# Kernel tuning notes

Measured on AMD Instinct MI355X. Metric: run time of the kernel, lower is better.

Reference implementation:

```python
import jax, jax.numpy as jnp
import numpy as np

NE, EW, TOP_K, T_D, MAXNNZ = 32, 2944, 4, 8, 256
ALPHA, LIMIT, ORIG = 1.702, 7.0, 2880
HID = 2048


def setup_inputs() -> dict:
    key = jax.random.key(0)
    ks = jax.random.split(key, 7)
    dt = jnp.float16
    hid = jax.random.normal(ks[0], (1, 1024, HID), dtype=dt)
    # rand_init() sets all params to torch.rand(...)/5 -> Uniform[0, 0.2)
    gate_w = (jax.random.uniform(ks[1], (NE, HID), dtype=dt) * 0.2).astype(dt)
    u = (jax.random.uniform(ks[2], (NE * EW, HID), dtype=dt) * 0.2).astype(dt)
    g = (jax.random.uniform(ks[3], (NE * EW, HID), dtype=dt) * 0.2).astype(dt)
    d = (jax.random.uniform(ks[4], (HID, NE * EW), dtype=dt) * 0.2).astype(dt)
    ub = (jax.random.uniform(ks[5], (NE * EW,), dtype=dt) * 0.2).astype(dt)
    gb = (jax.random.uniform(ks[6], (NE * EW,), dtype=dt) * 0.2).astype(dt)
    return {"hid": hid, "gate_w": gate_w, "u": u, "g": g, "d": d, "ub": ub, "gb": gb}


def _act(up, gate):
    # clamped GLU: gate clamped above, up clamped both sides; glu = g*sigmoid(alpha*g); (up+1)*glu
    gate = jnp.minimum(gate, LIMIT)
    up = jnp.clip(up, -LIMIT, LIMIT)
    glu = gate * jax.nn.sigmoid(gate * ALPHA)
    act = (up + 1.0) * glu
    return act.at[..., ORIG:].set(0)  # padded inter dims (2880..2944) zeroed


def _forward(hid, gate_w, u, g, d, ub, gb):
    B, S, H = hid.shape
    x = hid.reshape(-1, H)           # [bs, H]
    bs = x.shape[0]

    # --- routing: softmax -> top-k -> renormalize -> scatter to sparse weights ---
    logits = (x @ gate_w.T).astype(jnp.float32)          # [bs, NE]
    probs = jax.nn.softmax(logits, axis=1)
    vals, idx = jax.lax.top_k(probs, TOP_K)
    vals = vals / vals.sum(axis=1, keepdims=True)
    sparse_rw = jnp.zeros_like(probs).at[jnp.arange(bs)[:, None], idx].set(vals)
    rw = sparse_rw.astype(x.dtype)                        # [bs, NE]

    # --- expert selection: t_d dense experts + t_d sparse experts by load ---
    routing_n = jnp.count_nonzero(rw, axis=0)
    mask_c = jax.lax.top_k(routing_n, 2 * T_D)[1]         # [2*T_D]
    cd, cs = mask_c[:T_D], mask_c[T_D:]
    # top-MAXNNZ tokens per sparse expert
    mask_r = jax.lax.top_k(sparse_rw[:, cs].T, MAXNNZ)[1].T  # [MAXNNZ, T_D]

    U = u.reshape(NE, EW, H)
    G = g.reshape(NE, EW, H)
    UB = ub.reshape(NE, EW)
    GB = gb.reshape(NE, EW)
    D = d.reshape(H, NE, EW)

    # --- dense experts: every token runs through the t_d hottest experts ---
    up_d = jnp.einsum('nh,teh->nte', x, U[cd]) + UB[cd]   # [bs, T_D, EW]
    gt_d = jnp.einsum('nh,teh->nte', x, G[cd]) + GB[cd]
    act_d = _act(up_d, gt_d) * rw[:, cd][..., None]       # routing weight combine
    out = jnp.einsum('nte,hte->nh', act_d, D[:, cd])      # [bs, H]

    # --- sparse experts: gather top-MAXNNZ tokens, MLP, scatter-add back ---
    xs = x[mask_r]                                        # [M, T_D, H]
    up_s = jnp.einsum('mth,teh->mte', xs, U[cs]) + UB[cs]
    gt_s = jnp.einsum('mth,teh->mte', xs, G[cs]) + GB[cs]
    w_s = rw[mask_r, cs[None, :]]                         # [M, T_D]
    act_s = _act(up_s, gt_s) * w_s[..., None]
    contrib = jnp.einsum('mte,hte->mth', act_s, D[:, cs])  # [M, T_D, H]
    out = out.at[mask_r.reshape(-1)].add(contrib.reshape(-1, H))

    return out.reshape(B, S, H)


def reference(hid, gate_w, u, g, d, ub, gb):
    return _forward(hid, gate_w, u, g, d, ub, gb)
```

## Files before the change

kernel.cpp:

```cpp
#include <hip/hip_runtime.h>

#define HID 2048
#define NE_ 32
#define EW_ 2944
#define ORIG_ 2880
#define TOPK_ 4
#define MAXNNZ_ 256
#define BS_ 1024
#define NEWTOT (NE_*EW_)

typedef unsigned short u16;
typedef _Float16 h8  __attribute__((ext_vector_type(8)));
typedef float  f32x4 __attribute__((ext_vector_type(4)));
typedef float  fv4   __attribute__((ext_vector_type(4)));

__device__ __forceinline__ u16 f2h_bits(float f){
  union{ _Float16 h; u16 u; } c; c.h = (_Float16)f; return c.u;
}
__device__ __forceinline__ float f16q(float f){ return (float)(_Float16)f; }

__device__ __forceinline__ h8 cvt8(fv4 a, fv4 b){
  h8 r;
  r[0]=(_Float16)a[0]; r[1]=(_Float16)a[1]; r[2]=(_Float16)a[2]; r[3]=(_Float16)a[3];
  r[4]=(_Float16)b[0]; r[5]=(_Float16)b[1]; r[6]=(_Float16)b[2]; r[7]=(_Float16)b[3];
  return r;
}
__device__ __forceinline__ int ldsx(int row, int chunk){
  return row*32 + ((chunk ^ ((row>>1)&3))*8);
}

__device__ __forceinline__ void barrier_lgkm(){
  asm volatile("s_waitcnt lgkmcnt(0)" ::: "memory");
  __builtin_amdgcn_s_barrier();
  __builtin_amdgcn_sched_barrier(0);
}

__global__ __launch_bounds__(256) void k_xcvt(const float* __restrict__ x,
                                              u16* __restrict__ xh)
{
  const int base = (blockIdx.x*256 + threadIdx.x)*8;
  fv4 a = *(const fv4*)(x+base), b = *(const fv4*)(x+base+4);
  *(h8*)(xh+base) = cvt8(a,b);
}

__global__ __launch_bounds__(256) void k_gate(const float* __restrict__ x,
                                              const float* __restrict__ gw,
                                              float* __restrict__ rw,
                                              float* __restrict__ rwf,
                                              int* __restrict__ counts)
{
  __shared__ float slog[4][NE_];
  const int tid = threadIdx.x, wid = tid>>6, lane = tid&63;
  const int n = blockIdx.x*4 + wid;
  const float* xr = x + (size_t)n*HID + lane*32;
  float xf[32];
  #pragma unroll
  for (int i=0;i<8;i++){
    fv4 v = *(const fv4*)(xr + i*4);
    #pragma unroll
    for (int j=0;j<4;j++) xf[i*4+j] = v[j];
  }
  for (int e=0;e<NE_;e++){
    const float* gr = gw + (size_t)e*HID + lane*32;
    float p = 0.f;
    #pragma unroll
    for (int i=0;i<8;i++){
      fv4 v = *(const fv4*)(gr + i*4);
      #pragma unroll
      for (int j=0;j<4;j++) p += xf[i*4+j]*v[j];
    }
    #pragma unroll
    for (int s=32;s>0;s>>=1) p += __shfl_xor(p, s);
    if (lane==0) slog[wid][e] = f16q(p);
  }
  if (lane==0){
    float mx=-1e30f;
    for (int e=0;e<NE_;e++) mx = fmaxf(mx, slog[wid][e]);
    float pr[NE_]; float sum=0.f;
    for (int e=0;e<NE_;e++){ float v=__expf(slog[wid][e]-mx); pr[e]=v; sum+=v; }
    for (int e=0;e<NE_;e++) pr[e] = pr[e]/sum;
    int   idx[TOPK_]; float val[TOPK_]; bool used[NE_];
    for (int e=0;e<NE_;e++) used[e]=false;
    float vs=0.f;
    for (int k=0;k<TOPK_;k++){
      float best=-1.f; int bi=0;
      for (int e=0;e<NE_;e++) if(!used[e] && pr[e]>best){best=pr[e];bi=e;}
      used[bi]=true; idx[k]=bi; val[k]=best; vs+=best;
    }
    float* rwr  = rw  + (size_t)n*NE_;
    float* rwfr = rwf + (size_t)n*NE_;
    for (int k=0;k<TOPK_;k++){
      float vraw = val[k]/vs;
      float q = f16q(vraw);
      rwr[idx[k]]  = q;
      rwfr[idx[k]] = vraw;
      if (q!=0.f) atomicAdd(counts+idx[k], 1);
    }
  }
}

__global__ void k_rank(const int* __restrict__ counts, int* __restrict__ cdcs)
{
  if (threadIdx.x==0){
    int cnt[NE_]; bool used[NE_];
    for (int e=0;e<NE_;e++){ cnt[e]=counts[e]; used[e]=false; }
    for (int k=0;k<16;k++){
      int best=-1, bi=0;
      for (int e=0;e<NE_;e++) if(!used[e] && cnt[e]>best){best=cnt[e];bi=e;}
      used[bi]=true; cdcs[k]=bi;
    }
  }
}

__global__ __launch_bounds__(256) void k_lists(const float* __restrict__ rw,
                                               const float* __restrict__ rwf,
                                               const int* __restrict__ cdcs,
                                               int* __restrict__ tok_all,
                                               int* __restrict__ cnt_all,
                                               int* __restrict__ inv,
                                               int* __restrict__ invcnt)
{
  __shared__ float v[BS_];
  __shared__ int scnt;
  const int z = blockIdx.x;
  const int e = cdcs[z];
  const int tid = threadIdx.x;
  for (int i=tid;i<BS_;i+=256) tok_all[z*BS_+i] = 0;
  for (int i=tid;i<BS_;i+=256) v[i] = (z<8) ? rw[(size_t)i*NE_+e] : rwf[(size_t)i*NE_+e];
  if (tid==0) scnt = 0;
  __syncthreads();
  for (int i=tid;i<BS_;i+=256){
    bool take;
    if (z<8){
      take = (v[i]!=0.f);
    } else {
      float vi=v[i]; int r=0;
      for (int m=0;m<BS_;m++){
        float vm=v[m];
        r += (vm>vi) || (vm==vi && m<i);
      }
      take = (r<MAXNNZ_) && (rw[(size_t)i*NE_+e]!=0.f);
    }
    if (take){
      int slot = atomicAdd(&scnt,1);
      tok_all[z*BS_+slot] = i;
      int c = atomicAdd(&invcnt[i],1);
      inv[i*4+c] = (z<<16) | slot;
    }
  }
  __syncthreads();
  if (tid==0) cnt_all[z] = scnt;
}

__global__ __launch_bounds__(256, 3) void k_fused(const u16* __restrict__ xh,
                                               const float* __restrict__ uw,
                                               const float* __restrict__ gww,
                                               const float* __restrict__ ub,
                                               const float* __restrict__ gb,
                                               const float* __restrict__ rw,
                                               const int* __restrict__ cdcs,
                                               const int* __restrict__ tok_all,
                                               const int* __restrict__ cnt_all,
                                               u16* __restrict__ act)
{
  const int z=blockIdx.z, bx=blockIdx.x, by=blockIdx.y;
  const int cnt = cnt_all[z];
  if (by*256 >= cnt) return;
  const int e = cdcs[z];
  __shared__ __align__(16) u16 ldsA[2][256*32];
  __shared__ __align__(16) u16 ldsB[2][64*32];
  const int tid=threadIdx.x, lane=tid&63, w=tid>>6;
  const int ar = tid>>2, ach = tid&3;
  const u16* ap[4];
  #pragma unroll
  for (int r=0;r<4;r++){
    const int tok = tok_all[z*BS_ + by*256 + ar + r*64];
    ap[r] = xh + (size_t)tok*HID + ach*8;
  }
  const int br = ar;
  const float* bp = (br<32 ? uw  + ((size_t)e*EW_ + bx*32 + br)*HID
                           : gww + ((size_t)e*EW_ + bx*32 + (br-32))*HID) + ach*8;

  f32x4 au[4][2], ag[4][2];
  #pragma unroll
  for (int i=0;i<4;i++)
    #pragma unroll
    for (int j=0;j<2;j++)
      #pragma unroll
      for (int q=0;q<4;q++){ au[i][j][q]=0.f; ag[i][j][q]=0.f; }

  h8 As[4]; fv4 Ba, Bb;
  #pragma unroll
  for (int r=0;r<4;r++) As[r] = *(const h8*)ap[r];
  Ba = *(const fv4*)bp; Bb = *(const fv4*)(bp+4);

  const int NK = HID/32;
  #pragma unroll 2
  for (int kt=0; kt<NK; kt++){
    u16* A = ldsA[kt&1]; u16* B = ldsB[kt&1];
    #pragma unroll
    for (int r=0;r<4;r++) *(h8*)&A[ldsx(ar + r*64, ach)] = As[r];
    *(h8*)&B[ldsx(br, ach)] = cvt8(Ba,Bb);
    if (kt+1<NK){
      const int k1=(kt+1)*32;
      #pragma unroll
      for (int r=0;r<4;r++) As[r] = *(const h8*)(ap[r]+k1);
      Ba=*(const fv4*)(bp+k1); Bb=*(const fv4*)(bp+k1+4);
    }
    barrier_lgkm();
    const int kq = lane>>4;
    h8 af[4], fu[2], fg[2];
    #pragma unroll
    for (int m=0;m<4;m++) af[m] = *(const h8*)&A[ldsx(w*64+m*16+(lane&15), kq)];
    #pragma unroll
    for (int n2=0;n2<2;n2++){
      fu[n2] = *(const h8*)&B[ldsx(   n2*16+(lane&15), kq)];
      fg[n2] = *(const h8*)&B[ldsx(32+n2*16+(lane&15), kq)];
    }
    #pragma unroll
    for (int m=0;m<4;m++)
      #pragma unroll
      for (int n2=0;n2<2;n2++){
        au[m][n2]=__builtin_amdgcn_mfma_f32_16x16x32_f16(af[m],fu[n2],au[m][n2],0,0,0);
        ag[m][n2]=__builtin_amdgcn_mfma_f32_16x16x32_f16(af[m],fg[n2],ag[m][n2],0,0,0);
      }
  }

  #pragma unroll
  for (int n2=0;n2<2;n2++){
    const int col = bx*32 + n2*16 + (lane&15);
    const float ubv = ub[(size_t)e*EW_ + col];
    const float gbv = gb[(size_t)e*EW_ + col];
    #pragma unroll
    for (int m=0;m<4;m++){
      #pragma unroll
      for (int j=0;j<4;j++){
        const int s = by*256 + w*64 + m*16 + (lane>>4)*4 + j;
        if (s < cnt){
          float upv = f16q(au[m][n2][j] + ubv);
          float gtv = f16q(ag[m][n2][j] + gbv);
          float wv = rw[(size_t)tok_all[z*BS_+s]*NE_ + e];
          float gc = fminf(gtv, 7.0f);
          float uc = fminf(fmaxf(upv,-7.0f),7.0f);
          float glu = gc * (1.f/(1.f+__expf(-gc*1.702f)));
          act[((size_t)z*BS_+s)*ORIG_ + col] = f2h_bits((uc+1.f)*glu*wv);
        }
      }
    }
  }
}

__global__ __launch_bounds__(256, 3) void k_down(const u16* __restrict__ act,
                                              const float* __restrict__ dw,
                                              const int* __restrict__ cdcs,
                                              const int* __restrict__ cnt_all,
                                              u16* __restrict__ contrib)
{
  const int zz=blockIdx.z, bx=blockIdx.x, by=blockIdx.y;
  const int z = zz>>1, kh = zz&1;
  const int cnt = cnt_all[z];
  if (by*256 >= cnt) return;
  const int e = cdcs[z];
  __shared__ __align__(16) u16 ldsA[2][256*32];
  __shared__ __align__(16) u16 ldsB[2][64*32];
  const int tid=threadIdx.x, lane=tid&63, w=tid>>6;
  const int ar = tid>>2, ach = tid&3;
  const int kbase = kh*1440;

  const u16* ap[4];
  #pragma unroll
  for (int r=0;r<4;r++)
    ap[r] = act + ((size_t)z*BS_ + by*256 + ar + r*64)*ORIG_ + kbase + ach*8;
  const float* bp = dw + (size_t)(bx*64 + ar)*NEWTOT + (size_t)e*EW_ + kbase + ach*8;

  f32x4 acc[4][4];
  #pragma unroll
  for (int i=0;i<4;i++)
    #pragma unroll
    for (int j=0;j<4;j++)
      #pragma unroll
      for (int q=0;q<4;q++) acc[i][j][q]=0.f;

  h8 As[4]; fv4 Ba, Bb;
  #pragma unroll
  for (int r=0;r<4;r++) As[r] = *(const h8*)ap[r];
  Ba = *(const fv4*)bp; Bb = *(const fv4*)(bp+4);

  const int NK = 1440/32;
  #pragma unroll 2
  for (int kt=0; kt<NK; kt++){
    u16* A = ldsA[kt&1]; u16* B = ldsB[kt&1];
    #pragma unroll
    for (int r=0;r<4;r++) *(h8*)&A[ldsx(ar + r*64, ach)] = As[r];
    *(h8*)&B[ldsx(ar, ach)] = cvt8(Ba,Bb);
    if (kt+1<NK){
      const int k1 = (kt+1)*32;
      #pragma unroll
      for (int r=0;r<4;r++) As[r] = *(const h8*)(ap[r]+k1);
      Ba=*(const fv4*)(bp+k1); Bb=*(const fv4*)(bp+k1+4);
    }
    barrier_lgkm();
    const int kq = lane>>4;
    h8 af[4], bfr[4];
    #pragma unroll
    for (int m=0;m<4;m++)    af[m]  = *(const h8*)&A[ldsx(w*64+m*16+(lane&15), kq)];
    #pragma unroll
    for (int n2=0;n2<4;n2++) bfr[n2] = *(const h8*)&B[ldsx(n2*16+(lane&15), kq)];
    #pragma unroll
    for (int m=0;m<4;m++)
      #pragma unroll
      for (int n2=0;n2<4;n2++)
        acc[m][n2]=__builtin_amdgcn_mfma_f32_16x16x32_f16(af[m],bfr[n2],acc[m][n2],0,0,0);
  }

  #pragma unroll
  for (int m=0;m<4;m++){
    #pragma unroll
    for (int j=0;j<4;j++){
      const int slot = by*256 + w*64 + m*16 + (lane>>4)*4 + j;
      if (slot < cnt){
        #pragma unroll
        for (int n2=0;n2<4;n2++){
          const int col = bx*64 + n2*16 + (lane&15);
          contrib[((size_t)zz*BS_ + slot)*HID + col] = f2h_bits(acc[m][n2][j]);
        }
      }
    }
  }
}

__global__ __launch_bounds__(256) void k_combine(const u16* __restrict__ contrib,
                                                 const int* __restrict__ inv,
                                                 const int* __restrict__ invcnt,
                                                 float* __restrict__ out)
{
  const int gid = blockIdx.x*256 + threadIdx.x;
  const int base = gid*8;
  const int n = base >> 11;
  const int h = base & 2047;
  float acc[8];
  #pragma unroll
  for (int q=0;q<8;q++) acc[q]=0.f;
  const int c = invcnt[n];
  for (int j=0;j<c;j++){
    const int code = inv[n*4+j];
    const int z = code>>16;
    const int slot = code & 0xFFFF;
    const u16* p = contrib + ((size_t)(z*2)*BS_ + slot)*HID + h;
    h8 v0 = *(const h8*)p;
    h8 v1 = *(const h8*)(p + (size_t)BS_*HID);
    #pragma unroll
    for (int q=0;q<8;q++) acc[q] += (float)v0[q] + (float)v1[q];
  }
  fv4 o0, o1;
  #pragma unroll
  for (int q=0;q<4;q++){ o0[q]=acc[q]; o1[q]=acc[4+q]; }
  *(fv4*)(out + base) = o0;
  *(fv4*)(out + base + 4) = o1;
}

extern "C" void kernel_launch(void* const* d_in, const int* in_sizes, int n_in,
                              void* d_out, int out_size, void* d_ws, size_t ws_size,
                              hipStream_t stream)
{
  const float* x  = (const float*)d_in[0];
  const float* gw = (const float*)d_in[1];
  const float* u  = (const float*)d_in[2];
  const float* g  = (const float*)d_in[3];
  const float* dw = (const float*)d_in[4];
  const float* ub = (const float*)d_in[5];
  const float* gb = (const float*)d_in[6];

  char* ws = (char*)d_ws;
  size_t off = 0;
  auto alloc = [&](size_t bytes)->void*{ void* p = ws + off; off += (bytes + 255) & ~(size_t)255; return p; };
  float* rw     = (float*)alloc((size_t)BS_*NE_*4);
  float* rwf    = (float*)alloc((size_t)BS_*NE_*4);
  int*   counts = (int*)  alloc(NE_*4);
  int*   invcnt = (int*)  alloc(BS_*4);
  size_t zero_span = off;
  int*   cdcs   = (int*)  alloc(16*4);
  int*   cnt_all= (int*)  alloc(16*4);
  int*   tok_all= (int*)  alloc((size_t)16*BS_*4);
  int*   inv    = (int*)  alloc((size_t)BS_*4*4);
  u16*   xh     = (u16*)  alloc((size_t)BS_*HID*2);
  u16*   act    = (u16*)  alloc((size_t)16*BS_*ORIG_*2);
  u16*   contrib= (u16*)  alloc((size_t)32*BS_*HID*2);
  if (off > ws_size) return;

  hipMemsetAsync(ws, 0, zero_span, stream);

  k_xcvt <<<BS_*HID/(256*8), 256, 0, stream>>>(x, xh);
  k_gate <<<BS_/4, 256, 0, stream>>>(x, gw, rw, rwf, counts);
  k_rank <<<1,     64,  0, stream>>>(counts, cdcs);
  k_lists<<<16,    256, 0, stream>>>(rw, rwf, cdcs, tok_all, cnt_all, inv, invcnt);

  k_fused<<<dim3(ORIG_/32, 4, 16), 256, 0, stream>>>(xh, u, g, ub, gb, rw,
                                                     cdcs, tok_all, cnt_all, act);
  k_down <<<dim3(HID/64, 4, 32), 256, 0, stream>>>(act, dw, cdcs, cnt_all, contrib);
  k_combine<<<BS_*HID/(256*8), 256, 0, stream>>>(contrib, inv, invcnt, (float*)d_out);
}
```

Measured before the change: 573.9 us.

## Fuse x conversion into gate, fold ranking into lists, halve GEMM M-tiles

The fp16 conversion of x moves into the gating kernel, and the single-thread expert ranking kernel is folded into each k_lists block, which recomputes its own k-th expert. This removes two launches. The up/gate and down GEMM kernels drop from 256-row to 128-row token tiles, which doubles the grid's y dimension, halves LDS and accumulator use, and raises the launch-bounds occupancy hint from 3 to 4. In exchange, each weight tile is reloaded and converted from fp32 twice as often across the token tiles, which adds weight traffic.

Measured after the change: 658.7 us. 1.15x slower.

```diff
diff --git a/kernel.cpp b/kernel.cpp
--- a/kernel.cpp
+++ b/kernel.cpp
@@ -35,19 +35,24 @@
   __builtin_amdgcn_sched_barrier(0);
 }
 
-__global__ __launch_bounds__(256) void k_xcvt(const float* __restrict__ x,
-                                              u16* __restrict__ xh)
-{
-  const int base = (blockIdx.x*256 + threadIdx.x)*8;
-  fv4 a = *(const fv4*)(x+base), b = *(const fv4*)(x+base+4);
-  *(h8*)(xh+base) = cvt8(a,b);
+__device__ __forceinline__ int rank_kth(const int* counts, int kth){
+  int cnt[NE_]; bool used[NE_];
+  for (int e=0;e<NE_;e++){ cnt[e]=counts[e]; used[e]=false; }
+  int bi=0;
+  for (int k=0;k<=kth;k++){
+    int best=-1; bi=0;
+    for (int e=0;e<NE_;e++) if(!used[e] && cnt[e]>best){best=cnt[e];bi=e;}
+    used[bi]=true;
+  }
+  return bi;
 }
 
 __global__ __launch_bounds__(256) void k_gate(const float* __restrict__ x,
                                               const float* __restrict__ gw,
                                               float* __restrict__ rw,
                                               float* __restrict__ rwf,
-                                              int* __restrict__ counts)
+                                              int* __restrict__ counts,
+                                              u16* __restrict__ xh)
 {
   __shared__ float slog[4][NE_];
   const int tid = threadIdx.x, wid = tid>>6, lane = tid&63;
@@ -59,6 +64,13 @@
     fv4 v = *(const fv4*)(xr + i*4);
     #pragma unroll
     for (int j=0;j<4;j++) xf[i*4+j] = v[j];
+  }
+  #pragma unroll
+  for (int c=0;c<4;c++){
+    h8 hv;
+    #pragma unroll
+    for (int j=0;j<8;j++) hv[j] = (_Float16)xf[c*8+j];
+    *(h8*)(xh + (size_t)n*HID + lane*32 + c*8) = hv;
   }
   for (int e=0;e<NE_;e++){
     const float* gr = gw + (size_t)e*HID + lane*32;
@@ -99,22 +111,10 @@
   }
 }
 
-__global__ void k_rank(const int* __restrict__ counts, int* __restrict__ cdcs)
-{
-  if (threadIdx.x==0){
-    int cnt[NE_]; bool used[NE_];
-    for (int e=0;e<NE_;e++){ cnt[e]=counts[e]; used[e]=false; }
-    for (int k=0;k<16;k++){
-      int best=-1, bi=0;
-      for (int e=0;e<NE_;e++) if(!used[e] && cnt[e]>best){best=cnt[e];bi=e;}
-      used[bi]=true; cdcs[k]=bi;
-    }
-  }
-}
-
 __global__ __launch_bounds__(256) void k_lists(const float* __restrict__ rw,
                                                const float* __restrict__ rwf,
-                                               const int* __restrict__ cdcs,
+                                               const int* __restrict__ counts,
+                                               int* __restrict__ cdcs,
                                                int* __restrict__ tok_all,
                                                int* __restrict__ cnt_all,
                                                int* __restrict__ inv,
@@ -122,12 +122,19 @@
 {
   __shared__ float v[BS_];
   __shared__ int scnt;
+  __shared__ int e_sh;
   const int z = blockIdx.x;
-  const int e = cdcs[z];
   const int tid = threadIdx.x;
+  if (tid==0){
+    int e = rank_kth(counts, z);
+    e_sh = e;
+    cdcs[z] = e;
+    scnt = 0;
+  }
   for (int i=tid;i<BS_;i+=256) tok_all[z*BS_+i] = 0;
+  __syncthreads();
+  const int e = e_sh;
   for (int i=tid;i<BS_;i+=256) v[i] = (z<8) ? rw[(size_t)i*NE_+e] : rwf[(size_t)i*NE_+e];
-  if (tid==0) scnt = 0;
   __syncthreads();
   for (int i=tid;i<BS_;i+=256){
     bool take;
@@ -152,7 +159,7 @@
   if (tid==0) cnt_all[z] = scnt;
 }
 
-__global__ __launch_bounds__(256, 3) void k_fused(const u16* __restrict__ xh,
+__global__ __launch_bounds__(256, 4) void k_fused(const u16* __restrict__ xh,
                                                const float* __restrict__ uw,
                                                const float* __restrict__ gww,
                                                const float* __restrict__ ub,
@@ -165,60 +172,55 @@
 {
   const int z=blockIdx.z, bx=blockIdx.x, by=blockIdx.y;
   const int cnt = cnt_all[z];
-  if (by*256 >= cnt) return;
+  if (by*128 >= cnt) return;
   const int e = cdcs[z];
-  __shared__ __align__(16) u16 ldsA[2][256*32];
+  __shared__ __align__(16) u16 ldsA[2][128*32];
   __shared__ __align__(16) u16 ldsB[2][64*32];
   const int tid=threadIdx.x, lane=tid&63, w=tid>>6;
-  const int ar = tid>>2, ach = tid&3;
-  const u16* ap[4];
-  #pragma unroll
-  for (int r=0;r<4;r++){
-    const int tok = tok_all[z*BS_ + by*256 + ar + r*64];
-    ap[r] = xh + (size_t)tok*HID + ach*8;
-  }
-  const int br = ar;
+  const int lr = lane&15, kq = lane>>4;
+
+  const int ar = tid>>1, c0 = (tid&1)*2;
+  const int tokA = tok_all[z*BS_ + by*128 + ar];
+  const u16* ap = xh + (size_t)tokA*HID + c0*8;
+  const int br = tid>>2, bch = tid&3;
   const float* bp = (br<32 ? uw  + ((size_t)e*EW_ + bx*32 + br)*HID
-                           : gww + ((size_t)e*EW_ + bx*32 + (br-32))*HID) + ach*8;
-
-  f32x4 au[4][2], ag[4][2];
-  #pragma unroll
-  for (int i=0;i<4;i++)
+                           : gww + ((size_t)e*EW_ + bx*32 + (br-32))*HID) + bch*8;
+
+  f32x4 au[2][2], ag[2][2];
+  #pragma unroll
+  for (int i=0;i<2;i++)
     #pragma unroll
     for (int j=0;j<2;j++)
       #pragma unroll
       for (int q=0;q<4;q++){ au[i][j][q]=0.f; ag[i][j][q]=0.f; }
 
-  h8 As[4]; fv4 Ba, Bb;
-  #pragma unroll
-  for (int r=0;r<4;r++) As[r] = *(const h8*)ap[r];
+  h8 As0, As1; fv4 Ba, Bb;
+  As0 = *(const h8*)ap; As1 = *(const h8*)(ap+8);
   Ba = *(const fv4*)bp; Bb = *(const fv4*)(bp+4);
 
   const int NK = HID/32;
   #pragma unroll 2
   for (int kt=0; kt<NK; kt++){
     u16* A = ldsA[kt&1]; u16* B = ldsB[kt&1];
-    #pragma unroll
-    for (int r=0;r<4;r++) *(h8*)&A[ldsx(ar + r*64, ach)] = As[r];
-    *(h8*)&B[ldsx(br, ach)] = cvt8(Ba,Bb);
+    *(h8*)&A[ldsx(ar, c0  )] = As0;
+    *(h8*)&A[ldsx(ar, c0+1)] = As1;
+    *(h8*)&B[ldsx(br, bch)] = cvt8(Ba,Bb);
     if (kt+1<NK){
       const int k1=(kt+1)*32;
-      #pragma unroll
-      for (int r=0;r<4;r++) As[r] = *(const h8*)(ap[r]+k1);
+      As0 = *(const h8*)(ap+k1); As1 = *(const h8*)(ap+k1+8);
       Ba=*(const fv4*)(bp+k1); Bb=*(const fv4*)(bp+k1+4);
     }
     barrier_lgkm();
-    const int kq = lane>>4;
-    h8 af[4], fu[2], fg[2];
-    #pragma unroll
-    for (int m=0;m<4;m++) af[m] = *(const h8*)&A[ldsx(w*64+m*16+(lane&15), kq)];
+    h8 af[2], fu[2], fg[2];
+    #pragma unroll
+    for (int m=0;m<2;m++) af[m] = *(const h8*)&A[ldsx(w*32+m*16+lr, kq)];
     #pragma unroll
     for (int n2=0;n2<2;n2++){
-      fu[n2] = *(const h8*)&B[ldsx(   n2*16+(lane&15), kq)];
-      fg[n2] = *(const h8*)&B[ldsx(32+n2*16+(lane&15), kq)];
-    }
-    #pragma unroll
-    for (int m=0;m<4;m++)
+      fu[n2] = *(const h8*)&B[ldsx(   n2*16+lr, kq)];
+      fg[n2] = *(const h8*)&B[ldsx(32+n2*16+lr, kq)];
+    }
+    #pragma unroll
+    for (int m=0;m<2;m++)
       #pragma unroll
       for (int n2=0;n2<2;n2++){
         au[m][n2]=__builtin_amdgcn_mfma_f32_16x16x32_f16(af[m],fu[n2],au[m][n2],0,0,0);
@@ -228,14 +230,14 @@
 
   #pragma unroll
   for (int n2=0;n2<2;n2++){
-    const int col = bx*32 + n2*16 + (lane&15);
+    const int col = bx*32 + n2*16 + lr;
     const float ubv = ub[(size_t)e*EW_ + col];
     const float gbv = gb[(size_t)e*EW_ + col];
     #pragma unroll
-    for (int m=0;m<4;m++){
+    for (int m=0;m<2;m++){
       #pragma unroll
       for (int j=0;j<4;j++){
-        const int s = by*256 + w*64 + m*16 + (lane>>4)*4 + j;
+        const int s = by*128 + w*32 + m*16 + kq*4 + j;
         if (s < cnt){
           float upv = f16q(au[m][n2][j] + ubv);
           float gtv = f16q(ag[m][n2][j] + gbv);
@@ -250,7 +252,7 @@
   }
 }
 
-__global__ __launch_bounds__(256, 3) void k_down(const u16* __restrict__ act,
+__global__ __launch_bounds__(256, 4) void k_down(const u16* __restrict__ act,
                                               const float* __restrict__ dw,
                                               const int* __restrict__ cdcs,
                                               const int* __restrict__ cnt_all,
@@ -259,69 +261,65 @@
   const int zz=blockIdx.z, bx=blockIdx.x, by=blockIdx.y;
   const int z = zz>>1, kh = zz&1;
   const int cnt = cnt_all[z];
-  if (by*256 >= cnt) return;
+  if (by*128 >= cnt) return;
   const int e = cdcs[z];
-  __shared__ __align__(16) u16 ldsA[2][256*32];
+  __shared__ __align__(16) u16 ldsA[2][128*32];
   __shared__ __align__(16) u16 ldsB[2][64*32];
   const int tid=threadIdx.x, lane=tid&63, w=tid>>6;
-  const int ar = tid>>2, ach = tid&3;
+  const int lr = lane&15, kq = lane>>4;
   const int kbase = kh*1440;
 
-  const u16* ap[4];
-  #pragma unroll
-  for (int r=0;r<4;r++)
-    ap[r] = act + ((size_t)z*BS_ + by*256 + ar + r*64)*ORIG_ + kbase + ach*8;
-  const float* bp = dw + (size_t)(bx*64 + ar)*NEWTOT + (size_t)e*EW_ + kbase + ach*8;
-
-  f32x4 acc[4][4];
-  #pragma unroll
-  for (int i=0;i<4;i++)
+  const int ar = tid>>1, c0 = (tid&1)*2;
+  const u16* ap = act + ((size_t)z*BS_ + by*128 + ar)*ORIG_ + kbase + c0*8;
+  const int br = tid>>2, bch = tid&3;
+  const float* bp = dw + (size_t)(bx*64 + br)*NEWTOT + (size_t)e*EW_ + kbase + bch*8;
+
+  f32x4 acc[2][4];
+  #pragma unroll
+  for (int i=0;i<2;i++)
     #pragma unroll
     for (int j=0;j<4;j++)
       #pragma unroll
       for (int q=0;q<4;q++) acc[i][j][q]=0.f;
 
-  h8 As[4]; fv4 Ba, Bb;
-  #pragma unroll
-  for (int r=0;r<4;r++) As[r] = *(const h8*)ap[r];
+  h8 As0, As1; fv4 Ba, Bb;
+  As0 = *(const h8*)ap; As1 = *(const h8*)(ap+8);
   Ba = *(const fv4*)bp; Bb = *(const fv4*)(bp+4);
 
   const int NK = 1440/32;
   #pragma unroll 2
   for (int kt=0; kt<NK; kt++){
     u16* A = ldsA[kt&1]; u16* B = ldsB[kt&1];
-    #pragma unroll
-    for (int r=0;r<4;r++) *(h8*)&A[ldsx(ar + r*64, ach)] = As[r];
-    *(h8*)&B[ldsx(ar, ach)] = cvt8(Ba,Bb);
+    *(h8*)&A[ldsx(ar, c0  )] = As0;
+    *(h8*)&A[ldsx(ar, c0+1)] = As1;
+    *(h8*)&B[ldsx(br, bch)] = cvt8(Ba,Bb);
     if (kt+1<NK){
       const int k1 = (kt+1)*32;
-      #pragma unroll
-      for (int r=0;r<4;r++) As[r] = *(const h8*)(ap[r]+k1);
+      As0 = *(const h8*)(ap+k1); As1 = *(const h8*)(ap+k1+8);
       Ba=*(const fv4*)(bp+k1); Bb=*(const fv4*)(bp+k1+4);
     }
     barrier_lgkm();
-    const int kq = lane>>4;
-    h8 af[4], bfr[4];
-    #pragma unroll
-    for (int m=0;m<4;m++)    af[m]  = *(const h8*)&A[ldsx(w*64+m*16+(lane&15), kq)];
-    #pragma unroll
-    for (int n2=0;n2<4;n2++) bfr[n2] = *(const h8*)&B[ldsx(n2*16+(lane&15), kq)];
-    #pragma unroll
-    for (int m=0;m<4;m++)
+    h8 af[2], bfr[4];
+    #pragma unroll
+    for (int m=0;m<2;m++)    af[m]  = *(const h8*)&A[ldsx(w*32+m*16+lr, kq)];
+    #pragma unroll
+    for (int n2=0;n2<4;n2++) bfr[n2] = *(const h8*)&B[ldsx(n2*16+lr, kq)];
+    #pragma unroll
+    for (int m=0;m<2;m++)
       #pragma unroll
       for (int n2=0;n2<4;n2++)
         acc[m][n2]=__builtin_amdgcn_mfma_f32_16x16x32_f16(af[m],bfr[n2],acc[m][n2],0,0,0);
   }
 
   #pragma unroll
-  for (int m=0;m<4;m++){
+  for (int m=0;m<2;m++){
     #pragma unroll
     for (int j=0;j<4;j++){
-      const int slot = by*256 + w*64 + m*16 + (lane>>4)*4 + j;
+      const int slot = by*128 + w*32 + m*16 + kq*4 + j;
       if (slot < cnt){
         #pragma unroll
         for (int n2=0;n2<4;n2++){
-          const int col = bx*64 + n2*16 + (lane&15);
+          const int col = bx*64 + n2*16 + lr;
           contrib[((size_t)zz*BS_ + slot)*HID + col] = f2h_bits(acc[m][n2][j]);
         }
       }
@@ -390,13 +388,11 @@
 
   hipMemsetAsync(ws, 0, zero_span, stream);
 
-  k_xcvt <<<BS_*HID/(256*8), 256, 0, stream>>>(x, xh);
-  k_gate <<<BS_/4, 256, 0, stream>>>(x, gw, rw, rwf, counts);
-  k_rank <<<1,     64,  0, stream>>>(counts, cdcs);
-  k_lists<<<16,    256, 0, stream>>>(rw, rwf, cdcs, tok_all, cnt_all, inv, invcnt);
-
-  k_fused<<<dim3(ORIG_/32, 4, 16), 256, 0, stream>>>(xh, u, g, ub, gb, rw,
+  k_gate <<<BS_/4, 256, 0, stream>>>(x, gw, rw, rwf, counts, xh);
+  k_lists<<<16,    256, 0, stream>>>(rw, rwf, counts, cdcs, tok_all, cnt_all, inv, invcnt);
+
+  k_fused<<<dim3(ORIG_/32, 8, 16), 256, 0, stream>>>(xh, u, g, ub, gb, rw,
                                                      cdcs, tok_all, cnt_all, act);
-  k_down <<<dim3(HID/64, 4, 32), 256, 0, stream>>>(act, dw, cdcs, cnt_all, contrib);
+  k_down <<<dim3(HID/64, 8, 32), 256, 0, stream>>>(act, dw, cdcs, cnt_all, contrib);
   k_combine<<<BS_*HID/(256*8), 256, 0, stream>>>(contrib, inv, invcnt, (float*)d_out);
 }
```
